# Optimization experiments

Hardware: AMD Instinct MI355X
Metric: run time of the kernel (lower is better)

## Reference

```python
import jax, jax.numpy as jnp
import numpy as np

DIM = 768
B, H_DIM, W_DIM = 16, 64, 64
N = H_DIM * W_DIM
WEIGHT_BITS = 5
SHIFT_MIN = -(2 ** (WEIGHT_BITS - 1) - 2)  # -14
SHIFT_MAX = 0
INT_BITS, FRAC_BITS = 16, 16


def round_to_fixed(x):
    # DeepShift utils.round_to_fixed: floor-based fixed-point quantization
    delta = 2.0 ** (-FRAC_BITS)
    bound = 2.0 ** (INT_BITS - 1)
    return jnp.clip(jnp.floor(x / delta) * delta, -bound, bound - 1)


def setup_inputs() -> dict:
    key = jax.random.key(0)
    k1, k2, k3, k4 = jax.random.split(key, 4)
    x = jax.random.normal(k1, (B, N, DIM), dtype=jnp.float32)
    # shift / sign parameters of Conv2dShift, depthwise kernel [C, 1, 3, 3]
    shift = jax.random.uniform(k2, (DIM, 1, 3, 3), minval=float(SHIFT_MIN), maxval=0.0, dtype=jnp.float32)
    sign = jax.random.uniform(k3, (DIM, 1, 3, 3), minval=-1.0, maxval=1.0, dtype=jnp.float32)
    bias = jax.random.normal(k4, (DIM,), dtype=jnp.float32) * 0.01
    return {"x": x, "shift": shift, "sign": sign, "bias": bias, "H": H_DIM, "W": W_DIM}


def reference(x, shift, sign, bias, H, W):
    Bb, Nn, C = x.shape
    # weight = sign(round(sign_param)) * 2**round(clamp(shift, [-14, 0]))
    shift_r = jnp.round(jnp.clip(shift, SHIFT_MIN, SHIFT_MAX))
    sign_r = jnp.sign(jnp.round(sign))
    w = (2.0 ** shift_r) * sign_r  # [C, 1, 3, 3] power-of-two weights
    # fixed-point quantize activations and bias
    xq = round_to_fixed(x)
    bq = round_to_fixed(bias)
    # [B, N, C] -> [B, C, H, W]
    img = jnp.transpose(xq, (0, 2, 1)).reshape(Bb, C, H, W)
    out = jax.lax.conv_general_dilated(
        img, w,
        window_strides=(1, 1),
        padding=((1, 1), (1, 1)),
        dimension_numbers=("NCHW", "OIHW", "NCHW"),
        feature_group_count=C,
    )
    out = out + bq[None, :, None, None]
    # [B, C, H, W] -> [B, N, C]
    return jnp.transpose(out.reshape(Bb, C, Nn), (0, 2, 1))
```

## Files before the change

kernel.cpp:

```cpp
#include <hip/hip_runtime.h>


#define DIM 768
#define HD  64
#define WD  64
#define BD  16
#define TH  8
#define NPIX (HD * WD)

typedef float f32x4 __attribute__((ext_vector_type(4)));

__device__ __forceinline__ float qfix(float x) {
    float v = floorf(x * 65536.0f) * 1.52587890625e-05f;
    return fminf(fmaxf(v, -32768.0f), 32767.0f);
}

__device__ __forceinline__ float4 zero4() { return make_float4(0.f, 0.f, 0.f, 0.f); }

__device__ __forceinline__ float4 q4(float4 v) {
    v.x = qfix(v.x); v.y = qfix(v.y); v.z = qfix(v.z); v.w = qfix(v.w);
    return v;
}

__device__ __forceinline__ float4 fma4(float4 a, float4 b, float4 c) {
    c.x = fmaf(a.x, b.x, c.x);
    c.y = fmaf(a.y, b.y, c.y);
    c.z = fmaf(a.z, b.z, c.z);
    c.w = fmaf(a.w, b.w, c.w);
    return c;
}

__global__ void wprep_kernel(const float* __restrict__ shift,
                             const float* __restrict__ sgn,
                             const float* __restrict__ bias,
                             float* __restrict__ wbuf,
                             float* __restrict__ bbuf) {
    int i = blockIdx.x * 256 + threadIdx.x;
    if (i < DIM * 9) {
        int c = i / 9;
        int k = i - c * 9;
        float sr = rintf(fminf(fmaxf(shift[i], -14.0f), 0.0f));
        float g  = rintf(sgn[i]);
        float sg = (g > 0.0f) ? 1.0f : ((g < 0.0f) ? -1.0f : 0.0f);
        wbuf[k * DIM + c] = exp2f(sr) * sg;
    }
    if (i < DIM) bbuf[i] = qfix(bias[i]);
}

struct Row { float4 l, m, r; };

__device__ __forceinline__ Row load_row(const float* p, bool valid, bool wl, bool wr) {
    Row r;
    if (valid) {
        r.m = q4(*(const float4*)p);
        r.l = wl ? q4(*(const float4*)(p - DIM)) : zero4();
        r.r = wr ? q4(*(const float4*)(p + DIM)) : zero4();
    } else {
        r.l = zero4(); r.m = zero4(); r.r = zero4();
    }
    return r;
}

__global__ __launch_bounds__(192) void dwconv_kernel(
        const float* __restrict__ x,
        const float* __restrict__ wbuf,
        const float* __restrict__ bbuf,
        float* __restrict__ out) {
    const int c  = threadIdx.x * 4;
    const int w  = blockIdx.x;
    const int h0 = blockIdx.y * TH;
    const int b  = blockIdx.z;

    float4 wk[9];
    #pragma unroll
    for (int k = 0; k < 9; ++k)
        wk[k] = *(const float4*)(wbuf + k * DIM + c);
    const float4 bq = *(const float4*)(bbuf + c);

    const bool wl = (w > 0), wr = (w < WD - 1);
    const float* xb = x   + ((size_t)b * NPIX + w) * DIM + c;
    float*       ob = out + ((size_t)b * NPIX + w) * DIM + c;
    const long rowstride = (long)WD * DIM;

    Row r0 = load_row(xb + (long)(h0 - 1) * rowstride, h0 > 0, wl, wr);
    Row r1 = load_row(xb + (long)h0 * rowstride, true, wl, wr);

    #pragma unroll
    for (int hh = 0; hh < TH; ++hh) {
        const int h = h0 + hh;
        Row r2 = load_row(xb + (long)(h + 1) * rowstride, (h + 1) < HD, wl, wr);
        float4 acc = bq;
        acc = fma4(wk[0], r0.l, acc);
        acc = fma4(wk[1], r0.m, acc);
        acc = fma4(wk[2], r0.r, acc);
        acc = fma4(wk[3], r1.l, acc);
        acc = fma4(wk[4], r1.m, acc);
        acc = fma4(wk[5], r1.r, acc);
        acc = fma4(wk[6], r2.l, acc);
        acc = fma4(wk[7], r2.m, acc);
        acc = fma4(wk[8], r2.r, acc);
        f32x4 av; av.x = acc.x; av.y = acc.y; av.z = acc.z; av.w = acc.w;
        __builtin_nontemporal_store(av, (f32x4*)(ob + (long)h * rowstride));
        r0 = r1; r1 = r2;
    }
}

extern "C" void kernel_launch(void* const* d_in, const int* in_sizes, int n_in,
                              void* d_out, int out_size, void* d_ws, size_t ws_size,
                              hipStream_t stream) {
    const float* x     = (const float*)d_in[0];
    const float* shift = (const float*)d_in[1];
    const float* sgn   = (const float*)d_in[2];
    const float* bias  = (const float*)d_in[3];
    float* out  = (float*)d_out;
    float* wbuf = (float*)d_ws;
    float* bbuf = wbuf + 9 * DIM;

    wprep_kernel<<<(DIM * 9 + 255) / 256, 256, 0, stream>>>(shift, sgn, bias, wbuf, bbuf);

    dim3 grid(WD, HD / TH, BD);
    dwconv_kernel<<<grid, 192, 0, stream>>>(x, wbuf, bbuf, out);
}
```

Baseline: 381.9 us.

## Tile depthwise conv over 4 output columns per thread to reuse neighbor loads

Each thread now computes 4 adjacent width positions and 16 rows instead of 1 column and 8 rows, loading 6 columns per row so horizontal neighbors are shared. This cuts redundant global/L2 loads of neighboring pixels. The trade-offs are a smaller grid and higher register pressure, which may reduce occupancy and latency hiding.

```diff
diff --git a/kernel.cpp b/kernel.cpp
--- a/kernel.cpp
+++ b/kernel.cpp
@@ -5,7 +5,8 @@
 #define HD  64
 #define WD  64
 #define BD  16
-#define TH  8
+#define TW  4
+#define TH  16
 #define NPIX (HD * WD)
 
 typedef float f32x4 __attribute__((ext_vector_type(4)));
@@ -47,18 +48,13 @@
     if (i < DIM) bbuf[i] = qfix(bias[i]);
 }
 
-struct Row { float4 l, m, r; };
-
-__device__ __forceinline__ Row load_row(const float* p, bool valid, bool wl, bool wr) {
-    Row r;
-    if (valid) {
-        r.m = q4(*(const float4*)p);
-        r.l = wl ? q4(*(const float4*)(p - DIM)) : zero4();
-        r.r = wr ? q4(*(const float4*)(p + DIM)) : zero4();
-    } else {
-        r.l = zero4(); r.m = zero4(); r.r = zero4();
+__device__ __forceinline__ void load_row6(float4* r, const float* p,
+                                          bool rowvalid, bool lv, bool rv) {
+    #pragma unroll
+    for (int j = 0; j < 6; ++j) {
+        bool v = rowvalid && (j == 0 ? lv : (j == 5 ? rv : true));
+        r[j] = v ? q4(*(const float4*)(p + (j - 1) * DIM)) : zero4();
     }
-    return r;
 }
 
 __global__ __launch_bounds__(192) void dwconv_kernel(
@@ -67,7 +63,7 @@
         const float* __restrict__ bbuf,
         float* __restrict__ out) {
     const int c  = threadIdx.x * 4;
-    const int w  = blockIdx.x;
+    const int w0 = blockIdx.x * TW;
     const int h0 = blockIdx.y * TH;
     const int b  = blockIdx.z;
 
@@ -77,31 +73,44 @@
         wk[k] = *(const float4*)(wbuf + k * DIM + c);
     const float4 bq = *(const float4*)(bbuf + c);
 
-    const bool wl = (w > 0), wr = (w < WD - 1);
-    const float* xb = x   + ((size_t)b * NPIX + w) * DIM + c;
-    float*       ob = out + ((size_t)b * NPIX + w) * DIM + c;
+    const bool lv = (w0 > 0), rv = (w0 + TW < WD);
+    const float* xb = x   + ((size_t)b * NPIX + w0) * DIM + c;
+    float*       ob = out + ((size_t)b * NPIX + w0) * DIM + c;
     const long rowstride = (long)WD * DIM;
 
-    Row r0 = load_row(xb + (long)(h0 - 1) * rowstride, h0 > 0, wl, wr);
-    Row r1 = load_row(xb + (long)h0 * rowstride, true, wl, wr);
+    float4 r0[6], r1[6], r2[6];
+    load_row6(r0, xb + (long)(h0 - 1) * rowstride, h0 > 0, lv, rv);
+    load_row6(r1, xb + (long)h0 * rowstride, true, lv, rv);
 
     #pragma unroll
     for (int hh = 0; hh < TH; ++hh) {
         const int h = h0 + hh;
-        Row r2 = load_row(xb + (long)(h + 1) * rowstride, (h + 1) < HD, wl, wr);
-        float4 acc = bq;
-        acc = fma4(wk[0], r0.l, acc);
-        acc = fma4(wk[1], r0.m, acc);
-        acc = fma4(wk[2], r0.r, acc);
-        acc = fma4(wk[3], r1.l, acc);
-        acc = fma4(wk[4], r1.m, acc);
-        acc = fma4(wk[5], r1.r, acc);
-        acc = fma4(wk[6], r2.l, acc);
-        acc = fma4(wk[7], r2.m, acc);
-        acc = fma4(wk[8], r2.r, acc);
-        f32x4 av; av.x = acc.x; av.y = acc.y; av.z = acc.z; av.w = acc.w;
-        __builtin_nontemporal_store(av, (f32x4*)(ob + (long)h * rowstride));
-        r0 = r1; r1 = r2;
+        load_row6(r2, xb + (long)(h + 1) * rowstride, (h + 1) < HD, lv, rv);
+
+        float4 acc[TW];
+        #pragma unroll
+        for (int i = 0; i < TW; ++i) acc[i] = bq;
+
+        #pragma unroll
+        for (int kx = 0; kx < 3; ++kx) {
+            #pragma unroll
+            for (int i = 0; i < TW; ++i) {
+                acc[i] = fma4(wk[0 + kx], r0[i + kx], acc[i]);
+                acc[i] = fma4(wk[3 + kx], r1[i + kx], acc[i]);
+                acc[i] = fma4(wk[6 + kx], r2[i + kx], acc[i]);
+            }
+        }
+
+        #pragma unroll
+        for (int i = 0; i < TW; ++i) {
+            f32x4 av;
+            av.x = acc[i].x; av.y = acc[i].y; av.z = acc[i].z; av.w = acc[i].w;
+            __builtin_nontemporal_store(av,
+                (f32x4*)(ob + (long)h * rowstride + (long)i * DIM));
+        }
+
+        #pragma unroll
+        for (int j = 0; j < 6; ++j) { r0[j] = r1[j]; r1[j] = r2[j]; }
     }
 }
 
@@ -118,6 +127,6 @@
 
     wprep_kernel<<<(DIM * 9 + 255) / 256, 256, 0, stream>>>(shift, sgn, bias, wbuf, bbuf);
 
-    dim3 grid(WD, HD / TH, BD);
+    dim3 grid(WD / TW, HD / TH, BD);
     dwconv_kernel<<<grid, 192, 0, stream>>>(x, wbuf, bbuf, out);
 }
```

Result: no change. 386.6 us (+1.2%).
